# Optimization experiments

Hardware: AMD Instinct MI355X
Metric: run time of the kernel (lower is better)

The kernel has to match this reference:

```python
import jax, jax.numpy as jnp
import numpy as np

N_COARSE = 200000
N_FINE = 800000
E = 3200000
EP = 2400000
C_IN = 128
C_OUT = 64


def setup_inputs() -> dict:
    key = jax.random.key(0)
    ks = jax.random.split(key, 8)
    x = jax.random.normal(ks[0], (N_COARSE, C_IN), dtype=jnp.float32)
    edge_index = jax.random.randint(ks[1], (2, E), 0, N_COARSE, dtype=jnp.int64)
    edge_attr = jax.random.uniform(ks[2], (E, 1), dtype=jnp.float32)
    pool_src = jax.random.randint(ks[3], (EP,), 0, N_COARSE, dtype=jnp.int64)
    pool_dst = jax.random.randint(ks[4], (EP,), 0, N_FINE, dtype=jnp.int64)
    pool_edge_attr = jax.random.uniform(ks[5], (EP, 1), dtype=jnp.float32)
    scale = 1.0 / np.sqrt(C_IN)
    W_root = jax.random.normal(ks[6], (C_IN, C_OUT), dtype=jnp.float32) * scale
    W_nbr = jax.random.normal(ks[7], (C_IN, C_OUT), dtype=jnp.float32) * scale
    b = jnp.zeros((C_OUT,), dtype=jnp.float32)
    return {
        "x": x, "W_root": W_root, "W_nbr": W_nbr, "b": b,
        "edge_index": edge_index, "edge_attr": edge_attr,
        "pool_src": pool_src, "pool_dst": pool_dst,
        "pool_edge_attr": pool_edge_attr, "n_fine": N_FINE,
    }


def reference(x, W_root, W_nbr, b, edge_index, edge_attr, pool_src, pool_dst, pool_edge_attr, n_fine):
    # --- CustomGraphConvPointPoint ---
    # self term: [Nc, C_OUT]
    h = x @ W_root + b
    # neighbor messages: transform once, then gather per-edge and weight by edge_attr
    m = x @ W_nbr                      # [Nc, C_OUT]
    src, dst = edge_index[0], edge_index[1]
    msg = m[src] * edge_attr           # [E, C_OUT], edge_attr broadcasts over channels
    agg = jax.ops.segment_sum(msg, dst, num_segments=N_COARSE)  # [Nc, C_OUT]
    h = h + agg
    # --- CustomUnpooling: scatter coarse features to fine nodes, weighted ---
    fine_msg = h[pool_src] * pool_edge_attr                     # [EP, C_OUT]
    y = jax.ops.segment_sum(fine_msg, pool_dst, num_segments=n_fine)  # [Nf, C_OUT]
    return y
```

## Files before the change

kernel.cpp:

```cpp
#include <hip/hip_runtime.h>

#define CIN 128
#define COUT 64

__global__ __launch_bounds__(256) void gemm_hm_kernel(
        const float* __restrict__ x,
        const float* __restrict__ Wr,
        const float* __restrict__ Wn,
        const float* __restrict__ b,
        float* __restrict__ h,
        float* __restrict__ m,
        int n_coarse) {
    __shared__ float xs[32][CIN];
    const int rowBase = blockIdx.x * 32;

    if (rowBase + 32 <= n_coarse) {
        const float4* x4 = (const float4*)(x + (long long)rowBase * CIN);
        float4* xs4 = (float4*)&xs[0][0];
        for (int i = threadIdx.x; i < 32 * (CIN / 4); i += 256) xs4[i] = x4[i];
    } else {
        for (int i = threadIdx.x; i < 32 * CIN; i += 256) {
            int r = i / CIN, k = i % CIN;
            int row = rowBase + r;
            xs[r][k] = (row < n_coarse) ? x[(long long)row * CIN + k] : 0.f;
        }
    }
    __syncthreads();

    const int wv = threadIdx.x >> 6;
    const int c  = threadIdx.x & 63;
    const int r0 = wv * 8;

    float ah[8], am[8];
    const float bias = b[c];
#pragma unroll
    for (int j = 0; j < 8; ++j) { ah[j] = bias; am[j] = 0.f; }

    for (int k = 0; k < CIN; k += 4) {
        const float wr0 = Wr[(k + 0) * COUT + c];
        const float wr1 = Wr[(k + 1) * COUT + c];
        const float wr2 = Wr[(k + 2) * COUT + c];
        const float wr3 = Wr[(k + 3) * COUT + c];
        const float wn0 = Wn[(k + 0) * COUT + c];
        const float wn1 = Wn[(k + 1) * COUT + c];
        const float wn2 = Wn[(k + 2) * COUT + c];
        const float wn3 = Wn[(k + 3) * COUT + c];
#pragma unroll
        for (int j = 0; j < 8; ++j) {
            const float4 xv = *(const float4*)&xs[r0 + j][k];
            ah[j] = fmaf(xv.x, wr0, ah[j]);
            ah[j] = fmaf(xv.y, wr1, ah[j]);
            ah[j] = fmaf(xv.z, wr2, ah[j]);
            ah[j] = fmaf(xv.w, wr3, ah[j]);
            am[j] = fmaf(xv.x, wn0, am[j]);
            am[j] = fmaf(xv.y, wn1, am[j]);
            am[j] = fmaf(xv.z, wn2, am[j]);
            am[j] = fmaf(xv.w, wn3, am[j]);
        }
    }

#pragma unroll
    for (int j = 0; j < 8; ++j) {
        const int row = rowBase + r0 + j;
        if (row < n_coarse) {
            h[row * COUT + c] = ah[j];
            m[row * COUT + c] = am[j];
        }
    }
}

__global__ __launch_bounds__(256) void build_lists_kernel(
        const int* __restrict__ src,
        const int* __restrict__ dst,
        const float* __restrict__ w,
        int* __restrict__ head,
        int4* __restrict__ entries,
        int n) {
    const int e = blockIdx.x * 256 + threadIdx.x;
    if (e >= n) return;
    const int d = dst[e];
    const int prev = atomicExch(&head[d], e);
    entries[e] = make_int4(prev, src[e], __float_as_int(w[e]), 0);
}

__global__ __launch_bounds__(256) void edge_gather_kernel(
        const float* __restrict__ m,
        const int* __restrict__ head,
        const int4* __restrict__ entries,
        float* __restrict__ h,
        int n_rows) {
    const int row = blockIdx.x * 4 + (threadIdx.x >> 6);
    const int c = threadIdx.x & 63;
    if (row >= n_rows) return;
    float acc = 0.f;
    int e = head[row];
    while (e >= 0) {
        const int4 en = entries[e];
        acc += m[en.y * COUT + c] * __int_as_float(en.z);
        e = en.x;
    }
    h[row * COUT + c] += acc;
}

__global__ __launch_bounds__(256) void pool_gather_kernel(
        const float* __restrict__ h,
        const int* __restrict__ head,
        const int4* __restrict__ entries,
        float* __restrict__ y,
        int n_rows) {
    const int row = blockIdx.x * 4 + (threadIdx.x >> 6);
    const int c = threadIdx.x & 63;
    if (row >= n_rows) return;
    float acc = 0.f;
    int e = head[row];
    while (e >= 0) {
        const int4 en = entries[e];
        acc += h[en.y * COUT + c] * __int_as_float(en.z);
        e = en.x;
    }
    y[row * COUT + c] = acc;
}

extern "C" void kernel_launch(void* const* d_in, const int* in_sizes, int n_in,
                              void* d_out, int out_size, void* d_ws, size_t ws_size,
                              hipStream_t stream) {
    const float* x      = (const float*)d_in[0];
    const float* W_root = (const float*)d_in[1];
    const float* W_nbr  = (const float*)d_in[2];
    const float* b      = (const float*)d_in[3];
    const int*   eidx   = (const int*)d_in[4];
    const float* eattr  = (const float*)d_in[5];
    const int*   psrc   = (const int*)d_in[6];
    const int*   pdst   = (const int*)d_in[7];
    const float* pattr  = (const float*)d_in[8];

    const int n_coarse = in_sizes[0] / CIN;
    const int n_edges  = in_sizes[4] / 2;
    const int n_pool   = in_sizes[6];
    const int n_fine   = out_size / COUT;

    const int* esrc = eidx;
    const int* edst = eidx + n_edges;

    float* h = (float*)d_ws;
    float* m = h + (size_t)n_coarse * COUT;

    char* outb = (char*)d_out;
    int4* entries1 = (int4*)outb;
    int*  head1    = (int*)(outb + (size_t)n_edges * sizeof(int4));

    char* mb = (char*)m;
    int4* entries2 = (int4*)mb;
    int*  head2    = (int*)(mb + (size_t)n_pool * sizeof(int4));

    hipMemsetAsync(head1, 0xFF, (size_t)n_coarse * sizeof(int), stream);

    gemm_hm_kernel<<<(n_coarse + 31) / 32, 256, 0, stream>>>(x, W_root, W_nbr, b, h, m, n_coarse);

    build_lists_kernel<<<(n_edges + 255) / 256, 256, 0, stream>>>(
        esrc, edst, eattr, head1, entries1, n_edges);

    edge_gather_kernel<<<(n_coarse + 3) / 4, 256, 0, stream>>>(
        m, head1, entries1, h, n_coarse);

    hipMemsetAsync(head2, 0xFF, (size_t)n_fine * sizeof(int), stream);

    build_lists_kernel<<<(n_pool + 255) / 256, 256, 0, stream>>>(
        psrc, pdst, pattr, head2, entries2, n_pool);

    pool_gather_kernel<<<(n_fine + 3) / 4, 256, 0, stream>>>(
        h, head2, entries2, (float*)d_out, n_fine);
}
```

Baseline: 1.262 ms.

## Replace linked-list edge grouping with counting-sort CSR and unrolled gathers

Replaces the per-destination linked lists built with atomicExch with a CSR layout: a histogram of destinations, a block-scan with an atomic cursor to assign segment bases, and an atomic-fill scatter of packed (src*COUT, weight) pairs. The gather kernels then read contiguous edge ranges and unroll by four, removing the serial pointer-chasing dependency so several feature loads can be in flight at once. The cost is extra kernel launches and a second atomic pass over the edges. Segments are not globally ordered by row, which keeps the scan simple but loses some locality.

New measurement: 1.370 ms. 8.6% more time.

```diff
diff --git a/kernel.cpp b/kernel.cpp
--- a/kernel.cpp
+++ b/kernel.cpp
@@ -69,54 +69,111 @@
     }
 }
 
-__global__ __launch_bounds__(256) void build_lists_kernel(
-        const int* __restrict__ src,
-        const int* __restrict__ dst,
-        const float* __restrict__ w,
-        int* __restrict__ head,
-        int4* __restrict__ entries,
-        int n) {
+__global__ __launch_bounds__(256) void hist_kernel(
+        const int* __restrict__ dst, int* __restrict__ cnt, int n) {
+    const int e = blockIdx.x * 256 + threadIdx.x;
+    if (e < n) atomicAdd(&cnt[dst[e]], 1);
+}
+
+__global__ __launch_bounds__(256) void assign_base_kernel(
+        const int* __restrict__ cnt, int* __restrict__ base,
+        int* __restrict__ fill, int* __restrict__ cursor, int n) {
+    __shared__ int s[256];
+    __shared__ int blockBase;
+    const int tid = threadIdx.x;
+    const int i = blockIdx.x * 256 + tid;
+    const int v = (i < n) ? cnt[i] : 0;
+    s[tid] = v;
+    __syncthreads();
+#pragma unroll
+    for (int off = 1; off < 256; off <<= 1) {
+        int t = (tid >= off) ? s[tid - off] : 0;
+        __syncthreads();
+        if (tid >= off) s[tid] += t;
+        __syncthreads();
+    }
+    if (tid == 255) blockBase = atomicAdd(cursor, s[255]);
+    __syncthreads();
+    if (i < n) {
+        const int bse = blockBase + s[tid] - v;
+        base[i] = bse;
+        fill[i] = bse;
+    }
+}
+
+__global__ __launch_bounds__(256) void scatter_kernel(
+        const int* __restrict__ src, const int* __restrict__ dst,
+        const float* __restrict__ w, int* __restrict__ fill,
+        int2* __restrict__ edges, int n) {
     const int e = blockIdx.x * 256 + threadIdx.x;
     if (e >= n) return;
     const int d = dst[e];
-    const int prev = atomicExch(&head[d], e);
-    entries[e] = make_int4(prev, src[e], __float_as_int(w[e]), 0);
-}
-
-__global__ __launch_bounds__(256) void edge_gather_kernel(
+    const int pos = atomicAdd(&fill[d], 1);
+    edges[pos] = make_int2(src[e] * COUT, __float_as_int(w[e]));
+}
+
+__global__ __launch_bounds__(256) void csr_gather_add_kernel(
         const float* __restrict__ m,
-        const int* __restrict__ head,
-        const int4* __restrict__ entries,
-        float* __restrict__ h,
-        int n_rows) {
+        const int* __restrict__ base, const int* __restrict__ cnt,
+        const int2* __restrict__ edges,
+        float* __restrict__ h, int n_rows) {
     const int row = blockIdx.x * 4 + (threadIdx.x >> 6);
     const int c = threadIdx.x & 63;
     if (row >= n_rows) return;
+    const int p = base[row];
+    const int n = cnt[row];
     float acc = 0.f;
-    int e = head[row];
-    while (e >= 0) {
-        const int4 en = entries[e];
-        acc += m[en.y * COUT + c] * __int_as_float(en.z);
-        e = en.x;
+    int j = 0;
+    for (; j + 4 <= n; j += 4) {
+        const int2 e0 = edges[p + j + 0];
+        const int2 e1 = edges[p + j + 1];
+        const int2 e2 = edges[p + j + 2];
+        const int2 e3 = edges[p + j + 3];
+        const float v0 = m[e0.x + c];
+        const float v1 = m[e1.x + c];
+        const float v2 = m[e2.x + c];
+        const float v3 = m[e3.x + c];
+        acc = fmaf(v0, __int_as_float(e0.y), acc);
+        acc = fmaf(v1, __int_as_float(e1.y), acc);
+        acc = fmaf(v2, __int_as_float(e2.y), acc);
+        acc = fmaf(v3, __int_as_float(e3.y), acc);
+    }
+    for (; j < n; ++j) {
+        const int2 e0 = edges[p + j];
+        acc = fmaf(m[e0.x + c], __int_as_float(e0.y), acc);
     }
     h[row * COUT + c] += acc;
 }
 
-__global__ __launch_bounds__(256) void pool_gather_kernel(
+__global__ __launch_bounds__(256) void csr_gather_write_kernel(
         const float* __restrict__ h,
-        const int* __restrict__ head,
-        const int4* __restrict__ entries,
-        float* __restrict__ y,
-        int n_rows) {
+        const int* __restrict__ base, const int* __restrict__ cnt,
+        const int2* __restrict__ edges,
+        float* __restrict__ y, int n_rows) {
     const int row = blockIdx.x * 4 + (threadIdx.x >> 6);
     const int c = threadIdx.x & 63;
     if (row >= n_rows) return;
+    const int p = base[row];
+    const int n = cnt[row];
     float acc = 0.f;
-    int e = head[row];
-    while (e >= 0) {
-        const int4 en = entries[e];
-        acc += h[en.y * COUT + c] * __int_as_float(en.z);
-        e = en.x;
+    int j = 0;
+    for (; j + 4 <= n; j += 4) {
+        const int2 e0 = edges[p + j + 0];
+        const int2 e1 = edges[p + j + 1];
+        const int2 e2 = edges[p + j + 2];
+        const int2 e3 = edges[p + j + 3];
+        const float v0 = h[e0.x + c];
+        const float v1 = h[e1.x + c];
+        const float v2 = h[e2.x + c];
+        const float v3 = h[e3.x + c];
+        acc = fmaf(v0, __int_as_float(e0.y), acc);
+        acc = fmaf(v1, __int_as_float(e1.y), acc);
+        acc = fmaf(v2, __int_as_float(e2.y), acc);
+        acc = fmaf(v3, __int_as_float(e3.y), acc);
+    }
+    for (; j < n; ++j) {
+        const int2 e0 = edges[p + j];
+        acc = fmaf(h[e0.x + c], __int_as_float(e0.y), acc);
     }
     y[row * COUT + c] = acc;
 }
@@ -146,28 +203,36 @@
     float* m = h + (size_t)n_coarse * COUT;
 
     char* outb = (char*)d_out;
-    int4* entries1 = (int4*)outb;
-    int*  head1    = (int*)(outb + (size_t)n_edges * sizeof(int4));
-
-    char* mb = (char*)m;
-    int4* entries2 = (int4*)mb;
-    int*  head2    = (int*)(mb + (size_t)n_pool * sizeof(int4));
-
-    hipMemsetAsync(head1, 0xFF, (size_t)n_coarse * sizeof(int), stream);
+    int2* edges1  = (int2*)outb;
+    char* p1      = outb + (size_t)n_edges * sizeof(int2);
+    int*  cnt1    = (int*)p1;
+    int*  cursor1 = (int*)(p1 + (size_t)n_coarse * 4);
+    int*  base1   = (int*)(p1 + (size_t)n_coarse * 4 + 16);
+    int*  fill1   = (int*)(p1 + (size_t)n_coarse * 4 + 16 + (size_t)n_coarse * 4);
+
+    char* mb      = (char*)m;
+    int2* edges2  = (int2*)mb;
+    char* p2      = mb + (size_t)n_pool * sizeof(int2);
+    int*  cnt2    = (int*)p2;
+    int*  cursor2 = (int*)(p2 + (size_t)n_fine * 4);
+    int*  base2   = (int*)(p2 + (size_t)n_fine * 4 + 16);
+    int*  fill2   = (int*)(p2 + (size_t)n_fine * 4 + 16 + (size_t)n_fine * 4);
 
     gemm_hm_kernel<<<(n_coarse + 31) / 32, 256, 0, stream>>>(x, W_root, W_nbr, b, h, m, n_coarse);
 
-    build_lists_kernel<<<(n_edges + 255) / 256, 256, 0, stream>>>(
-        esrc, edst, eattr, head1, entries1, n_edges);
-
-    edge_gather_kernel<<<(n_coarse + 3) / 4, 256, 0, stream>>>(
-        m, head1, entries1, h, n_coarse);
-
-    hipMemsetAsync(head2, 0xFF, (size_t)n_fine * sizeof(int), stream);
-
-    build_lists_kernel<<<(n_pool + 255) / 256, 256, 0, stream>>>(
-        psrc, pdst, pattr, head2, entries2, n_pool);
-
-    pool_gather_kernel<<<(n_fine + 3) / 4, 256, 0, stream>>>(
-        h, head2, entries2, (float*)d_out, n_fine);
-}
+    hipMemsetAsync(cnt1, 0, (size_t)n_coarse * 4 + 16, stream);
+    hist_kernel<<<(n_edges + 255) / 256, 256, 0, stream>>>(edst, cnt1, n_edges);
+    assign_base_kernel<<<(n_coarse + 255) / 256, 256, 0, stream>>>(cnt1, base1, fill1, cursor1, n_coarse);
+    scatter_kernel<<<(n_edges + 255) / 256, 256, 0, stream>>>(esrc, edst, eattr, fill1, edges1, n_edges);
+
+    csr_gather_add_kernel<<<(n_coarse + 3) / 4, 256, 0, stream>>>(
+        m, base1, cnt1, edges1, h, n_coarse);
+
+    hipMemsetAsync(cnt2, 0, (size_t)n_fine * 4 + 16, stream);
+    hist_kernel<<<(n_pool + 255) / 256, 256, 0, stream>>>(pdst, cnt2, n_pool);
+    assign_base_kernel<<<(n_fine + 255) / 256, 256, 0, stream>>>(cnt2, base2, fill2, cursor2, n_fine);
+    scatter_kernel<<<(n_pool + 255) / 256, 256, 0, stream>>>(psrc, pdst, pattr, fill2, edges2, n_pool);
+
+    csr_gather_write_kernel<<<(n_fine + 3) / 4, 256, 0, stream>>>(
+        h, base2, cnt2, edges2, (float*)d_out, n_fine);
+}
```
